# Kernel tuning notes

Hardware: AMD Instinct MI355X
Metric: run time of the kernel (lower is better)

The kernel has to match this reference:

```python
import jax, jax.numpy as jnp
import numpy as np
import math

H_IMG, W_IMG = 800, 1216
STRIDES = [4, 8, 16, 32, 64]
SIZES = [32, 64, 128, 256, 512]
RATIOS = [0.5, 1.0, 2.0]
NUM_PER_LEVEL = [(-(-H_IMG // s)) * (-(-W_IMG // s)) * len(RATIOS) for s in STRIDES]
A_TOTAL = sum(NUM_PER_LEVEL)  # 728973
B = 4
PRE_NMS = 1000   # pre_nms_top_n['testing']
POST_NMS = 1000  # post_nms_top_n['testing']
NMS_TH = 0.7
MIN_SIZE = 1e-3
BBOX_XFORM_CLIP = math.log(1000.0 / 16)
NEG = -1e10
LEVELS_NP = np.repeat(np.arange(len(NUM_PER_LEVEL)), NUM_PER_LEVEL).astype(np.int32)


def _make_anchors():
    out = []
    for stride, size in zip(STRIDES, SIZES):
        fh, fw = -(-H_IMG // stride), -(-W_IMG // stride)
        r = np.sqrt(np.asarray(RATIOS, dtype=np.float64))
        ws, hs = size / r, size * r
        base = np.stack([-ws / 2, -hs / 2, ws / 2, hs / 2], axis=1)  # [3,4]
        sx = np.arange(fw, dtype=np.float64) * stride
        sy = np.arange(fh, dtype=np.float64) * stride
        gy, gx = np.meshgrid(sy, sx, indexing='ij')
        shifts = np.stack([gx.ravel(), gy.ravel(), gx.ravel(), gy.ravel()], axis=1)
        out.append((shifts[:, None, :] + base[None]).reshape(-1, 4))
    return np.concatenate(out, 0).astype(np.float32)


def setup_inputs() -> dict:
    key = jax.random.key(0)
    k1, k2 = jax.random.split(key)
    objectness = jax.random.normal(k1, (B, A_TOTAL), dtype=jnp.float32)
    deltas = jax.random.normal(k2, (B, A_TOTAL, 4), dtype=jnp.float32) * 0.2
    anchors = jnp.asarray(_make_anchors())
    return {'objectness': objectness, 'deltas': deltas, 'anchors': anchors}


def _decode(deltas, anchors):
    # BoxCoder.decode with weights (1,1,1,1)
    wa = anchors[:, 2] - anchors[:, 0]
    ha = anchors[:, 3] - anchors[:, 1]
    cxa = anchors[:, 0] + 0.5 * wa
    cya = anchors[:, 1] + 0.5 * ha
    dx, dy = deltas[..., 0], deltas[..., 1]
    dw = jnp.minimum(deltas[..., 2], BBOX_XFORM_CLIP)
    dh = jnp.minimum(deltas[..., 3], BBOX_XFORM_CLIP)
    cx = dx * wa + cxa
    cy = dy * ha + cya
    w = jnp.exp(dw) * wa
    h = jnp.exp(dh) * ha
    return jnp.stack([cx - 0.5 * w, cy - 0.5 * h, cx + 0.5 * w, cy + 0.5 * h], axis=-1)


def _topk_per_level(obj):
    # _get_top_n_idx: independent top-k within each anchor level, indices offset
    idxs, off = [], 0
    for n in NUM_PER_LEVEL:
        k = min(PRE_NMS, n)
        _, ti = jax.lax.top_k(obj[:, off:off + n], k)
        idxs.append(ti + off)
        off += n
    return jnp.concatenate(idxs, axis=1)


def _pairwise_iou(b):
    area = (b[:, 2] - b[:, 0]) * (b[:, 3] - b[:, 1])
    lt = jnp.maximum(b[:, None, :2], b[None, :, :2])
    rb = jnp.minimum(b[:, None, 2:], b[None, :, 2:])
    wh = jnp.clip(rb - lt, 0.0)
    inter = wh[..., 0] * wh[..., 1]
    return inter / (area[:, None] + area[None, :] - inter)


def _filter_image(boxes, scores, lvl):
    # clip_boxes_to_image
    x1 = jnp.clip(boxes[:, 0], 0.0, W_IMG)
    y1 = jnp.clip(boxes[:, 1], 0.0, H_IMG)
    x2 = jnp.clip(boxes[:, 2], 0.0, W_IMG)
    y2 = jnp.clip(boxes[:, 3], 0.0, H_IMG)
    boxes = jnp.stack([x1, y1, x2, y2], axis=1)
    # remove_small_boxes (as a validity mask; fixed shapes under jit)
    valid = ((x2 - x1) >= MIN_SIZE) & ((y2 - y1) >= MIN_SIZE)
    scores = jnp.where(valid, scores, NEG)
    N = boxes.shape[0]
    # batched_nms: offset boxes per level so levels never overlap
    sg_boxes = jax.lax.stop_gradient(boxes)
    offset = lvl.astype(boxes.dtype) * (sg_boxes.max() + 1.0)
    order = jnp.argsort(-jax.lax.stop_gradient(scores))
    iou = _pairwise_iou(sg_boxes[order] + offset[order][:, None])  # [N,N]
    idx = jnp.arange(N)
    def body(i, keep):
        sup = (iou[i] > NMS_TH) & keep[i] & (idx > i)
        return keep & ~sup
    keep = jax.lax.fori_loop(0, N, body, valid[order])
    # kept entries in score order, then truncate to POST_NMS (fixed shape)
    prio = jnp.where(keep, idx, N)
    sel = jnp.argsort(prio)[:POST_NMS]
    kept = keep[sel]
    src = order[sel]
    out_b = jnp.where(kept[:, None], boxes[src], 0.0)
    out_s = jnp.where(kept, scores[src], NEG)
    return out_b, out_s


def reference(objectness, deltas, anchors):
    proposals = _decode(deltas, anchors)                      # [B,A,4]
    top_idx = _topk_per_level(objectness)                     # [B,5000]
    obj_sel = jnp.take_along_axis(objectness, top_idx, axis=1)
    prop_sel = jnp.take_along_axis(proposals, top_idx[..., None], axis=1)
    lvl_sel = jnp.asarray(LEVELS_NP)[top_idx]
    boxes, scores = jax.vmap(_filter_image)(prop_sel, obj_sel, lvl_sel)
    return boxes, scores  # [B,POST_NMS,4], [B,POST_NMS]
```

## Files before the change

### kernel.cpp

```cpp
#include <hip/hip_runtime.h>
#include <stdint.h>

#pragma clang fp contract(off)

#define B_IMGS   4
#define NLVL     5
#define A_TOTAL  242991
#define NSEL     4741
#define NBUCK    8192
#define BSHIFT   19
#define CAND_CAP 2048
#define POST_NMS 1000
#define NBL      (B_IMGS * NLVL)
#define NMS_TH   0.7f
#define NEGV     (-1e10f)
#define W_IMGF   1216.0f
#define H_IMGF   800.0f
#define MIN_SZ   1e-3f
#define BBOX_CLIP 4.135166556742356f

#define NSLICE_PER_IMG 34

__device__ __forceinline__ int lvl_k(int l) { return (l == 4) ? 741 : 1000; }

__device__ __forceinline__ unsigned flipf(float f) {
    unsigned u = __float_as_uint(f);
    return u ^ (unsigned)(((int)u >> 31) | 0x80000000);
}
__device__ __forceinline__ float unflipf(unsigned os) {
    unsigned u = (os & 0x80000000u) ? (os ^ 0x80000000u) : ~os;
    return __uint_as_float(u);
}

__device__ __forceinline__ void async_cp16(const void* g, void* l) {
    __builtin_amdgcn_global_load_lds(
        (const __attribute__((address_space(1))) unsigned*)g,
        (__attribute__((address_space(3))) unsigned*)l,
        16, 0, 0);
}

static constexpr size_t OFF_BM    = 0;
static constexpr size_t OFF_CNT   = 128;
static constexpr size_t OFF_DI    = 208;
static constexpr size_t OFF_D2    = 224;
static constexpr size_t OFF_HSL   = 256;
static constexpr size_t OFF_PSL   = OFF_HSL  + (size_t)B_IMGS * NSLICE_PER_IMG * NBUCK * 4;
static constexpr size_t OFF_CAND  = OFF_PSL  + (size_t)B_IMGS * NSLICE_PER_IMG * 256 * 4;
static constexpr size_t OFF_SEL   = OFF_CAND + (size_t)NBL * CAND_CAP * 8;
static constexpr size_t OFF_BOXR  = OFF_SEL  + (size_t)B_IMGS * NSEL * 8;
static constexpr size_t OFF_SCR   = OFF_BOXR + (size_t)B_IMGS * NSEL * 16;
static constexpr size_t OFF_BOXL  = OFF_SCR  + (size_t)B_IMGS * NSEL * 4;
static constexpr size_t OFF_VAL   = OFF_BOXL + (size_t)B_IMGS * NSEL * 16;
static constexpr size_t OFF_RMAP  = OFF_VAL  + (size_t)B_IMGS * NSEL * 4;
static constexpr size_t OFF_KEEP  = OFF_RMAP + (size_t)B_IMGS * NSEL * 4;
static constexpr size_t OFF_MASK  = (OFF_KEEP + (size_t)B_IMGS * NSEL * 4 + 15) & ~(size_t)15;
static constexpr size_t WS_NEED   = OFF_MASK + (size_t)NBL * 1024 * 16 * 8;

#define HBLK_PER_IMG 34
__global__ __launch_bounds__(512) void k_hist(const float* __restrict__ obj,
                                              unsigned* __restrict__ hist_sl,
                                              unsigned* __restrict__ part_sl,
                                              unsigned* __restrict__ cntz) {
    __shared__ __align__(16) unsigned lh[NBUCK];
    const int tid = threadIdx.x;
    const int b = blockIdx.x / HBLK_PER_IMG;
    const int r = blockIdx.x - b * HBLK_PER_IMG;
    if (r == 33) {
        if (b == 0 && tid < 28) cntz[tid] = 0;
        return;
    }
    int sofs, sub, chunk, lstart, n;
    if (r < 24)      { sofs = 0;  sub = r;      chunk = 7600; lstart = 0;      n = 182400; }
    else if (r < 30) { sofs = 24; sub = r - 24; chunk = 7600; lstart = 182400; n = 45600; }
    else if (r < 32) { sofs = 30; sub = r - 30; chunk = 5700; lstart = 228000; n = 11400; }
    else             { sofs = 32; sub = 0;      chunk = 2850; lstart = 239400; n = 2850; }
    #pragma unroll
    for (int i = tid; i < NBUCK; i += 512) lh[i] = 0;
    __syncthreads();
    const int s0 = sub * chunk;
    const int m = min(chunk, n - s0);
    const float* src = obj + (size_t)b * A_TOTAL + lstart + s0;
    const int peel0 = (int)(((16u - ((unsigned)(uintptr_t)src & 15u)) & 15u) >> 2);
    const int peel  = (peel0 < m) ? peel0 : m;
    const int nv    = (m - peel) >> 2;
    const float4* s4 = (const float4*)(src + peel);
    const int tail0 = peel + (nv << 2);
#define H1(f) atomicAdd(&lh[flipf(f) >> BSHIFT], 1u)
#define H4(v) do { H1((v).x); H1((v).y); H1((v).z); H1((v).w); } while (0)
    if (tid < peel) H1(src[tid]);
    for (int i = tid; i < nv; i += 2048) {
        if (i + 1536 < nv) {
            float4 a0 = s4[i], a1 = s4[i + 512], a2 = s4[i + 1024], a3 = s4[i + 1536];
            H4(a0); H4(a1); H4(a2); H4(a3);
        } else {
            float4 a0 = s4[i]; H4(a0);
            if (i + 512  < nv) { float4 a = s4[i + 512];  H4(a); }
            if (i + 1024 < nv) { float4 a = s4[i + 1024]; H4(a); }
        }
    }
    for (int i = tail0 + tid; i < m; i += 512) H1(src[i]);
#undef H4
#undef H1
    __syncthreads();
    const int slice = b * NSLICE_PER_IMG + sofs + sub;
    unsigned* gh = hist_sl + (size_t)slice * NBUCK;
    #pragma unroll
    for (int i = tid; i < NBUCK / 4; i += 512)
        ((uint4*)gh)[i] = ((const uint4*)lh)[i];
    if (tid < 256) {
        unsigned s = 0;
        #pragma unroll
        for (int i = 0; i < 32; ++i) s += lh[tid * 32 + ((i + tid) & 31)];
        part_sl[(size_t)slice * 256 + tid] = s;
    }
}

#define CBLK_PER_IMG 65
__global__ __launch_bounds__(256) void k_compact(const float* __restrict__ obj,
                                                 const unsigned* __restrict__ hist_sl,
                                                 const unsigned* __restrict__ part_sl,
                                                 unsigned* __restrict__ cnt,
                                                 unsigned long long* __restrict__ cand) {
    __shared__ unsigned long long sbuf[CAND_CAP];
    __shared__ unsigned wsum[4];
    __shared__ unsigned fcnt[4];
    __shared__ unsigned s_cum, s_thr, lcnt, gbase;
    const int tid = threadIdx.x;
    const int b = blockIdx.x / CBLK_PER_IMG;
    const int r = blockIdx.x - b * CBLK_PER_IMG;
    int l, sofs, nsub, sub, chunk, lstart, n;
    if (r < 48)      { l = 0; sofs = 0;  nsub = 24; sub = r;      chunk = 3800; lstart = 0;      n = 182400; }
    else if (r < 60) { l = 1; sofs = 24; nsub = 6;  sub = r - 48; chunk = 3800; lstart = 182400; n = 45600; }
    else if (r < 63) { l = 2; sofs = 30; nsub = 2;  sub = r - 60; chunk = 3800; lstart = 228000; n = 11400; }
    else if (r == 63){ l = 3; sofs = 32; nsub = 1;  sub = 0;      chunk = 2850; lstart = 239400; n = 2850; }
    else             { l = 4; sofs = 33; nsub = 0;  sub = 0;      chunk = 741;  lstart = 242250; n = 741; }
    const int bl = b * NLVL + l;
    const int kl = lvl_k(l);
    if (tid == 0) { lcnt = 0; s_cum = 0; }
    __syncthreads();
    unsigned T = 0;
    if (l < 4) {
        const int lane = tid & 63, wv = tid >> 6;
        const unsigned* pb = part_sl + (size_t)(b * NSLICE_PER_IMG + sofs) * 256 + (255 - tid);
        unsigned x = 0;
        #pragma unroll 6
        for (int s = 0; s < nsub; ++s) x += pb[(size_t)s * 256];
        #pragma unroll
        for (int d = 1; d < 64; d <<= 1) {
            unsigned up = __shfl_up(x, d);
            if (lane >= d) x += up;
        }
        if (lane == 63) wsum[wv] = x;
        __syncthreads();
        unsigned add = 0;
        #pragma unroll
        for (int u = 0; u < 3; ++u) if (u < wv) add += wsum[u];
        const unsigned suffix = x + add;
        unsigned long long bm = __ballot(suffix >= (unsigned)kl);
        if (lane == 0) fcnt[wv] = (unsigned)__popcll(bm);
        __syncthreads();
        const int chnk = (int)(fcnt[0] + fcnt[1] + fcnt[2] + fcnt[3]) - 1;
        if ((255 - tid) == chnk + 1) s_cum = suffix;
        __syncthreads();
        if (tid < 64) {
            unsigned y = 0;
            if (tid < 32) {
                const unsigned* hb = hist_sl + (size_t)(b * NSLICE_PER_IMG + sofs) * NBUCK
                                   + chnk * 32 + (31 - tid);
                #pragma unroll 6
                for (int s = 0; s < nsub; ++s) y += hb[(size_t)s * NBUCK];
            }
            #pragma unroll
            for (int d = 1; d < 32; d <<= 1) {
                unsigned up = __shfl_up(y, d);
                if (tid >= d) y += up;
            }
            unsigned suf2 = s_cum + y;
            unsigned long long bm2 = __ballot((tid < 32) && (suf2 >= (unsigned)kl));
            if (tid == 0) {
                int istar = (int)__popcll(bm2) - 1;
                s_thr = (unsigned)(chnk * 32 + istar);
            }
        }
        __syncthreads();
        T = s_thr;
    }
    const int s0 = sub * chunk;
    const int m = min(chunk, n - s0);
    const int abase = lstart + s0;
    const float* src = obj + (size_t)b * A_TOTAL + abase;
    const int peel0 = (int)(((16u - ((unsigned)(uintptr_t)src & 15u)) & 15u) >> 2);
    const int peel  = (peel0 < m) ? peel0 : m;
    const int nv    = (m - peel) >> 2;
    const float4* s4 = (const float4*)(src + peel);
    const int tail0 = peel + (nv << 2);
#define E1(f, idx) do { unsigned os_ = flipf(f); \
    if ((os_ >> BSHIFT) >= T) { \
        unsigned slot = atomicAdd(&lcnt, 1u); \
        if (slot < CAND_CAP) \
            sbuf[slot] = (((unsigned long long)(~os_)) << 32) | (unsigned)(idx); \
    } } while (0)
#define E4(v, gb) do { E1((v).x, (gb)); E1((v).y, (gb) + 1); \
                       E1((v).z, (gb) + 2); E1((v).w, (gb) + 3); } while (0)
    if (tid < peel) E1(src[tid], abase + tid);
    for (int i = tid; i < nv; i += 512) {
        const int gb0 = abase + peel + (i << 2);
        if (i + 256 < nv) {
            float4 a0 = s4[i], a1 = s4[i + 256];
            E4(a0, gb0);
            E4(a1, gb0 + 1024);
        } else {
            float4 a0 = s4[i];
            E4(a0, gb0);
        }
    }
    for (int i = tail0 + tid; i < m; i += 256) E1(src[i], abase + i);
#undef E4
#undef E1
    __syncthreads();
    unsigned total = lcnt; if (total > CAND_CAP) total = CAND_CAP;
    if (tid == 0) gbase = atomicAdd(&cnt[bl], total);
    __syncthreads();
    const unsigned gb = gbase;
    for (unsigned i = tid; i < total; i += 256) {
        unsigned g = gb + i;
        if (g < CAND_CAP)
            cand[(size_t)bl * CAND_CAP + g] = sbuf[i];
    }
}

__device__ __forceinline__ int lbound_lds(const unsigned long long* s, int len,
                                          unsigned long long key) {
    int lo = 0, hi = len;
    while (lo < hi) {
        int mid = (lo + hi) >> 1;
        if (s[mid] < key) lo = mid + 1; else hi = mid;
    }
    return lo;
}

__global__ __launch_bounds__(1024) void k_sortdec(
        const unsigned long long* __restrict__ cand, const unsigned* __restrict__ cnt,
        unsigned long long* __restrict__ sel,
        const float* __restrict__ deltas, const float* __restrict__ anchors,
        float* __restrict__ boxes_r, float* __restrict__ score_r,
        float* __restrict__ boxes_l, int* __restrict__ valid_l,
        int* __restrict__ rankmap, float* __restrict__ boxmax,
        unsigned* __restrict__ done_i) {
    __shared__ __align__(16) char smem[38016];
    __shared__ float wmax[16];
    __shared__ int s_last;
    const int bl = blockIdx.x;
    const int b = bl / NLVL, l = bl - (bl / NLVL) * NLVL;
    const int tid = threadIdx.x;

    {
        unsigned long long* keys = (unsigned long long*)smem;
        int m = (int)cnt[bl];
        if (m > CAND_CAP) m = CAND_CAP;
        for (int i = tid; i < CAND_CAP; i += 1024)
            keys[i] = (i < m) ? cand[(size_t)bl * CAND_CAP + i] : ~0ULL;
        __syncthreads();
        for (int k = 2; k <= CAND_CAP; k <<= 1) {
            for (int j = k >> 1; j > 0; j >>= 1) {
                int i = ((tid / j) * (j << 1)) + (tid % j);
                int p = i + j;
                bool up = ((i & k) == 0);
                unsigned long long a = keys[i], c = keys[p];
                if ((a > c) == up) { keys[i] = c; keys[p] = a; }
                __syncthreads();
            }
        }
        int kl = lvl_k(l);
        for (int q = tid; q < kl; q += 1024)
            sel[(size_t)b * NSEL + l * 1000 + q] = keys[q];
    }
    __syncthreads();
    if (tid == 0) {
        __threadfence();
        unsigned old = __hip_atomic_fetch_add(done_i + b, 1u,
                                              __ATOMIC_ACQ_REL, __HIP_MEMORY_SCOPE_AGENT);
        s_last = (old == NLVL - 1);
        if (old == NLVL - 1) __threadfence();
    }
    __syncthreads();
    if (!s_last) return;

    unsigned long long* skey = (unsigned long long*)smem;
    for (int i = tid; i < NSEL; i += 1024)
        skey[i] = sel[(size_t)b * NSEL + i];
    __syncthreads();
    float mxall = 0.0f;
    for (int sub = 0; sub < 5; ++sub) {
        int p = sub * 1024 + tid;
        bool on = p < NSEL;
        float mx = 0.0f;
        if (on) {
            int l2i = p / 1000;
            int q = p - l2i * 1000;
            unsigned long long key = skey[p];
            unsigned a = (unsigned)(key & 0xFFFFFFFFu);
            unsigned os = ~((unsigned)(key >> 32));
            if (a >= A_TOTAL) a = 0;
            float score = unflipf(os);
            int r = q;
            for (int l2 = 0; l2 < NLVL; ++l2) {
                if (l2 == l2i) continue;
                r += lbound_lds(skey + l2 * 1000, lvl_k(l2), key);
            }
            const float* dv = deltas + ((size_t)b * A_TOTAL + a) * 4;
            const float* av = anchors + (size_t)a * 4;
            float ax1 = av[0], ay1 = av[1], ax2 = av[2], ay2 = av[3];
            float wa = ax2 - ax1, ha = ay2 - ay1;
            float cxa = ax1 + 0.5f * wa, cya = ay1 + 0.5f * ha;
            float dx = dv[0], dy = dv[1];
            float dw = fminf(dv[2], BBOX_CLIP), dh = fminf(dv[3], BBOX_CLIP);
            float cx = dx * wa + cxa, cy = dy * ha + cya;
            float w = expf(dw) * wa, h = expf(dh) * ha;
            float x1 = cx - 0.5f * w, y1 = cy - 0.5f * h;
            float x2 = cx + 0.5f * w, y2 = cy + 0.5f * h;
            float x1c = fminf(fmaxf(x1, 0.0f), W_IMGF);
            float y1c = fminf(fmaxf(y1, 0.0f), H_IMGF);
            float x2c = fminf(fmaxf(x2, 0.0f), W_IMGF);
            float y2c = fminf(fmaxf(y2, 0.0f), H_IMGF);
            int valid = ((x2c - x1c) >= MIN_SZ) && ((y2c - y1c) >= MIN_SZ);
            mx = fmaxf(fmaxf(x1c, y1c), fmaxf(x2c, y2c));
            size_t rp = (size_t)b * NSEL + r;
            boxes_r[rp * 4 + 0] = x1c; boxes_r[rp * 4 + 1] = y1c;
            boxes_r[rp * 4 + 2] = x2c; boxes_r[rp * 4 + 3] = y2c;
            score_r[rp] = score;
            size_t pp = (size_t)b * NSEL + p;
            boxes_l[pp * 4 + 0] = x1c; boxes_l[pp * 4 + 1] = y1c;
            boxes_l[pp * 4 + 2] = x2c; boxes_l[pp * 4 + 3] = y2c;
            valid_l[pp] = valid;
            rankmap[pp] = r;
        }
        mxall = fmaxf(mxall, mx);
    }
    #pragma unroll
    for (int o = 32; o > 0; o >>= 1)
        mxall = fmaxf(mxall, __shfl_xor(mxall, o));
    if ((tid & 63) == 0) wmax[tid >> 6] = mxall;
    __syncthreads();
    if (tid == 0) {
        float m2 = wmax[0];
        #pragma unroll
        for (int i = 1; i < 16; ++i) m2 = fmaxf(m2, wmax[i]);
        boxmax[b] = m2;
    }
}

__global__ void k_mask(const float* __restrict__ boxes_l, const float* __restrict__ boxmax,
                       unsigned long long* __restrict__ mask) {
    int bl = blockIdx.z;
    int b = bl / NLVL, l = bl - b * NLVL;
    int kl = lvl_k(l);
    int w = blockIdx.x, rg = blockIdx.y, tid = threadIdx.x;
    if (rg * 256 >= kl) return;
    float M = boxmax[b] + 1.0f;
    float off = (float)l * M;
    __shared__ float cb[64][5];
    int j0 = w * 64;
    if (tid < 64) {
        int j = j0 + tid;
        if (j < kl) {
            const float* bp = boxes_l + ((size_t)b * NSEL + l * 1000 + j) * 4;
            float x1 = bp[0] + off, y1 = bp[1] + off, x2 = bp[2] + off, y2 = bp[3] + off;
            cb[tid][0] = x1; cb[tid][1] = y1; cb[tid][2] = x2; cb[tid][3] = y2;
            cb[tid][4] = (x2 - x1) * (y2 - y1);
        }
    }
    __syncthreads();
    int i = rg * 256 + tid;
    if (i >= kl) return;
    unsigned long long word = 0;
    if (j0 + 63 > i) {
        const float* bp = boxes_l + ((size_t)b * NSEL + l * 1000 + i) * 4;
        float ix1 = bp[0] + off, iy1 = bp[1] + off, ix2 = bp[2] + off, iy2 = bp[3] + off;
        float ai = (ix2 - ix1) * (iy2 - iy1);
        int jmax = min(64, kl - j0);
        for (int bb = 0; bb < jmax; ++bb) {
            int jj = j0 + bb;
            if (jj <= i) continue;
            float ltx = fmaxf(ix1, cb[bb][0]), lty = fmaxf(iy1, cb[bb][1]);
            float rbx = fminf(ix2, cb[bb][2]), rby = fminf(iy2, cb[bb][3]);
            float ww = fmaxf(rbx - ltx, 0.0f), hh = fmaxf(rby - lty, 0.0f);
            float inter = ww * hh;
            float iou = inter / ((ai + cb[bb][4]) - inter);
            if (iou > NMS_TH) word |= (1ULL << bb);
        }
    }
    mask[((size_t)bl * 1024 + i) * 16 + w] = word;
}

__global__ __launch_bounds__(256) void k_resout(const int* __restrict__ valid_l,
                                                const int* __restrict__ rankmap,
                                                const unsigned long long* __restrict__ mask,
                                                int* __restrict__ keep_r,
                                                unsigned* __restrict__ done2,
                                                const float* __restrict__ boxes_r,
                                                const float* __restrict__ score_r,
                                                float* __restrict__ out) {
    __shared__ __align__(16) unsigned long long sbufA[64 * 16];
    __shared__ __align__(16) unsigned long long sbufB[64 * 16];
    __shared__ int ps[256];
    __shared__ int s_flag;
    const int bl = blockIdx.x;
    const int b = bl / NLVL, l = bl - b * NLVL;
    const int kl = lvl_k(l);
    const int tid = threadIdx.x;
    const int lane = tid & 63;
    const int base = b * NSEL + l * 1000;
    const int nch = (kl + 63) >> 6;
    const char* mbyte = (const char*)(mask + (size_t)bl * 1024 * 16);

    unsigned long long keep_w = 0;
    if (tid < 64) {
        for (int c = 0; c < 16; ++c) {
            int q = c * 64 + lane;
            int vv = (q < kl) ? valid_l[base + q] : 0;
            unsigned long long bm = __ballot(vv);
            if (lane == c) keep_w = bm;
        }
        const char* g0 = mbyte + (size_t)lane * 16;
        #pragma unroll
        for (int j = 0; j < 8; ++j)
            async_cp16(g0 + j * 1024, (char*)sbufA + j * 1024);
    }
    for (int c = 0; c < nch; ++c) {
        __syncthreads();
        if (tid < 64) {
            unsigned long long* cur = (c & 1) ? sbufB : sbufA;
            unsigned long long* nxt = (c & 1) ? sbufA : sbufB;
            if (c + 1 < nch) {
                const char* g1 = mbyte + (size_t)(c + 1) * 8192 + (size_t)lane * 16;
                #pragma unroll
                for (int j = 0; j < 8; ++j)
                    async_cp16(g1 + j * 1024, (char*)nxt + j * 1024);
            }
            unsigned long long kw = __shfl(keep_w, c);
            if (kw) {
                unsigned long long diag = cur[lane * 16 + c];
                unsigned dlo = (unsigned)diag, dhi = (unsigned)(diag >> 32);
                unsigned long long nz = __ballot(diag != 0ULL);
                unsigned long long rem = kw & nz;
                while (rem) {
                    int rr = __ffsll((long long)rem) - 1;
                    unsigned lo = __builtin_amdgcn_readlane(dlo, rr);
                    unsigned hi = __builtin_amdgcn_readlane(dhi, rr);
                    unsigned long long d = ((unsigned long long)hi << 32) | lo;
                    kw &= ~d;
                    rem &= ~(d | (1ULL << rr));
                }
                unsigned long long supp = 0;
                if (lane < 16) {
                    #pragma unroll
                    for (int rr = 0; rr < 64; ++rr) {
                        unsigned long long mm = cur[rr * 16 + lane];
                        supp |= (((kw >> rr) & 1ULL) ? mm : 0ULL);
                    }
                }
                if (lane == c) keep_w = kw;
                else if (lane < 16 && lane > c) keep_w &= ~supp;
            }
        }
    }
    __syncthreads();
    if (tid < 64) {
        for (int c = 0; c < 16; ++c) {
            unsigned long long kwc = __shfl(keep_w, c);
            int q = c * 64 + lane;
            if (q < kl)
                keep_r[b * NSEL + rankmap[base + q]] = (int)((kwc >> lane) & 1ULL);
        }
    }
    __syncthreads();

    if (tid == 0) {
        __threadfence();
        unsigned old = __hip_atomic_fetch_add(done2 + b, 1u,
                                              __ATOMIC_ACQ_REL, __HIP_MEMORY_SCOPE_AGENT);
        s_flag = (old == NLVL - 1);
        if (old == NLVL - 1) __threadfence();
    }
    __syncthreads();
    if (!s_flag) return;

    float* ob = out + (size_t)b * POST_NMS * 4;
    float* osc = out + (size_t)B_IMGS * POST_NMS * 4 + (size_t)b * POST_NMS;
    for (int p = tid; p < POST_NMS; p += 256) {
        ob[p * 4 + 0] = 0.0f; ob[p * 4 + 1] = 0.0f;
        ob[p * 4 + 2] = 0.0f; ob[p * 4 + 3] = 0.0f;
        osc[p] = NEGV;
    }
    __syncthreads();
    const int CH = 19;
    int basei = tid * CH;
    int c0 = 0;
    #pragma unroll
    for (int k = 0; k < CH; ++k) {
        int rr = basei + k;
        if (rr < NSEL) c0 += keep_r[b * NSEL + rr];
    }
    ps[tid] = c0;
    __syncthreads();
    for (int ofs = 1; ofs < 256; ofs <<= 1) {
        int v = (tid >= ofs) ? ps[tid - ofs] : 0;
        __syncthreads();
        ps[tid] += v;
        __syncthreads();
    }
    int p = ps[tid] - c0;
    #pragma unroll
    for (int k = 0; k < CH; ++k) {
        int rr = basei + k;
        if (rr < NSEL && keep_r[b * NSEL + rr]) {
            if (p < POST_NMS) {
                const float* bp = boxes_r + ((size_t)b * NSEL + rr) * 4;
                ob[p * 4 + 0] = bp[0]; ob[p * 4 + 1] = bp[1];
                ob[p * 4 + 2] = bp[2]; ob[p * 4 + 3] = bp[3];
                osc[p] = score_r[(size_t)b * NSEL + rr];
            }
            ++p;
        }
    }
}

extern "C" void kernel_launch(void* const* d_in, const int* in_sizes, int n_in,
                              void* d_out, int out_size, void* d_ws, size_t ws_size,
                              hipStream_t stream) {
    const float* obj     = (const float*)d_in[0];
    const float* deltas  = (const float*)d_in[1];
    const float* anchors = (const float*)d_in[2];
    float* out = (float*)d_out;

    char* ws = (char*)d_ws;
    float*               boxmax  = (float*)(ws + OFF_BM);
    unsigned*            cnt     = (unsigned*)(ws + OFF_CNT);
    unsigned*            done_i  = (unsigned*)(ws + OFF_DI);
    unsigned*            done2   = (unsigned*)(ws + OFF_D2);
    unsigned*            hist_sl = (unsigned*)(ws + OFF_HSL);
    unsigned*            part_sl = (unsigned*)(ws + OFF_PSL);
    unsigned long long*  cand    = (unsigned long long*)(ws + OFF_CAND);
    unsigned long long*  sel     = (unsigned long long*)(ws + OFF_SEL);
    float*               boxes_r = (float*)(ws + OFF_BOXR);
    float*               score_r = (float*)(ws + OFF_SCR);
    float*               boxes_l = (float*)(ws + OFF_BOXL);
    int*                 valid_l = (int*)(ws + OFF_VAL);
    int*                 rankmap = (int*)(ws + OFF_RMAP);
    int*                 keep_r  = (int*)(ws + OFF_KEEP);
    unsigned long long*  maskp   = (unsigned long long*)(ws + OFF_MASK);

    (void)in_sizes; (void)n_in; (void)out_size; (void)ws_size; (void)WS_NEED;

    k_hist<<<B_IMGS * HBLK_PER_IMG, 512, 0, stream>>>(obj, hist_sl, part_sl, cnt);
    k_compact<<<B_IMGS * CBLK_PER_IMG, 256, 0, stream>>>(obj, hist_sl, part_sl, cnt, cand);
    k_sortdec<<<NBL, 1024, 0, stream>>>(cand, cnt, sel, deltas, anchors,
                                        boxes_r, score_r, boxes_l, valid_l,
                                        rankmap, boxmax, done_i);
    k_mask<<<dim3(16, 4, NBL), 256, 0, stream>>>(boxes_l, boxmax, maskp);
    k_resout<<<NBL, 256, 0, stream>>>(valid_l, rankmap, maskp, keep_r, done2,
                                      boxes_r, score_r, out);
}
```

Before: 193.0 us.

## Replace last-block decode with per-image spin barrier splitting decode across five blocks

Before, only the last of the five level blocks per image did the ranking and decode of all ~4741 selected candidates, with five passes per thread. Now all five blocks wait on a per-image spin barrier and each decodes one 1024-wide slice. The per-image box max is written as five partials that k_mask reduces. This relies on all 20 blocks being co-resident for the spin barrier, and on the barrier counter being reset between calls, which is not visible here.

```diff
diff --git a/kernel.cpp b/kernel.cpp
--- a/kernel.cpp
+++ b/kernel.cpp
@@ -39,7 +39,7 @@
         16, 0, 0);
 }
 
-static constexpr size_t OFF_BM    = 0;
+static constexpr size_t OFF_BM5   = 0;
 static constexpr size_t OFF_CNT   = 128;
 static constexpr size_t OFF_DI    = 208;
 static constexpr size_t OFF_D2    = 224;
@@ -245,11 +245,10 @@
         const float* __restrict__ deltas, const float* __restrict__ anchors,
         float* __restrict__ boxes_r, float* __restrict__ score_r,
         float* __restrict__ boxes_l, int* __restrict__ valid_l,
-        int* __restrict__ rankmap, float* __restrict__ boxmax,
-        unsigned* __restrict__ done_i) {
+        int* __restrict__ rankmap, unsigned* __restrict__ boxmax5,
+        unsigned* __restrict__ bar_i) {
     __shared__ __align__(16) char smem[38016];
     __shared__ float wmax[16];
-    __shared__ int s_last;
     const int bl = blockIdx.x;
     const int b = bl / NLVL, l = bl - (bl / NLVL) * NLVL;
     const int tid = threadIdx.x;
@@ -276,88 +275,89 @@
             sel[(size_t)b * NSEL + l * 1000 + q] = keys[q];
     }
     __syncthreads();
+
     if (tid == 0) {
         __threadfence();
-        unsigned old = __hip_atomic_fetch_add(done_i + b, 1u,
-                                              __ATOMIC_ACQ_REL, __HIP_MEMORY_SCOPE_AGENT);
-        s_last = (old == NLVL - 1);
-        if (old == NLVL - 1) __threadfence();
-    }
-    __syncthreads();
-    if (!s_last) return;
+        __hip_atomic_fetch_add(bar_i + b, 1u, __ATOMIC_RELAXED, __HIP_MEMORY_SCOPE_AGENT);
+        while (__hip_atomic_load(bar_i + b, __ATOMIC_RELAXED, __HIP_MEMORY_SCOPE_AGENT)
+               < (unsigned)NLVL)
+            __builtin_amdgcn_s_sleep(2);
+        __threadfence();
+    }
+    __syncthreads();
 
     unsigned long long* skey = (unsigned long long*)smem;
     for (int i = tid; i < NSEL; i += 1024)
         skey[i] = sel[(size_t)b * NSEL + i];
     __syncthreads();
-    float mxall = 0.0f;
-    for (int sub = 0; sub < 5; ++sub) {
-        int p = sub * 1024 + tid;
-        bool on = p < NSEL;
-        float mx = 0.0f;
-        if (on) {
-            int l2i = p / 1000;
-            int q = p - l2i * 1000;
-            unsigned long long key = skey[p];
-            unsigned a = (unsigned)(key & 0xFFFFFFFFu);
-            unsigned os = ~((unsigned)(key >> 32));
-            if (a >= A_TOTAL) a = 0;
-            float score = unflipf(os);
-            int r = q;
-            for (int l2 = 0; l2 < NLVL; ++l2) {
-                if (l2 == l2i) continue;
-                r += lbound_lds(skey + l2 * 1000, lvl_k(l2), key);
-            }
-            const float* dv = deltas + ((size_t)b * A_TOTAL + a) * 4;
-            const float* av = anchors + (size_t)a * 4;
-            float ax1 = av[0], ay1 = av[1], ax2 = av[2], ay2 = av[3];
-            float wa = ax2 - ax1, ha = ay2 - ay1;
-            float cxa = ax1 + 0.5f * wa, cya = ay1 + 0.5f * ha;
-            float dx = dv[0], dy = dv[1];
-            float dw = fminf(dv[2], BBOX_CLIP), dh = fminf(dv[3], BBOX_CLIP);
-            float cx = dx * wa + cxa, cy = dy * ha + cya;
-            float w = expf(dw) * wa, h = expf(dh) * ha;
-            float x1 = cx - 0.5f * w, y1 = cy - 0.5f * h;
-            float x2 = cx + 0.5f * w, y2 = cy + 0.5f * h;
-            float x1c = fminf(fmaxf(x1, 0.0f), W_IMGF);
-            float y1c = fminf(fmaxf(y1, 0.0f), H_IMGF);
-            float x2c = fminf(fmaxf(x2, 0.0f), W_IMGF);
-            float y2c = fminf(fmaxf(y2, 0.0f), H_IMGF);
-            int valid = ((x2c - x1c) >= MIN_SZ) && ((y2c - y1c) >= MIN_SZ);
-            mx = fmaxf(fmaxf(x1c, y1c), fmaxf(x2c, y2c));
-            size_t rp = (size_t)b * NSEL + r;
-            boxes_r[rp * 4 + 0] = x1c; boxes_r[rp * 4 + 1] = y1c;
-            boxes_r[rp * 4 + 2] = x2c; boxes_r[rp * 4 + 3] = y2c;
-            score_r[rp] = score;
-            size_t pp = (size_t)b * NSEL + p;
-            boxes_l[pp * 4 + 0] = x1c; boxes_l[pp * 4 + 1] = y1c;
-            boxes_l[pp * 4 + 2] = x2c; boxes_l[pp * 4 + 3] = y2c;
-            valid_l[pp] = valid;
-            rankmap[pp] = r;
-        }
-        mxall = fmaxf(mxall, mx);
+    const int sub = l;
+    int p = sub * 1024 + tid;
+    bool on = p < NSEL;
+    float mx = 0.0f;
+    if (on) {
+        int l2i = p / 1000;
+        int q = p - l2i * 1000;
+        unsigned long long key = skey[p];
+        unsigned a = (unsigned)(key & 0xFFFFFFFFu);
+        unsigned os = ~((unsigned)(key >> 32));
+        if (a >= A_TOTAL) a = 0;
+        float score = unflipf(os);
+        int r = q;
+        for (int l2 = 0; l2 < NLVL; ++l2) {
+            if (l2 == l2i) continue;
+            r += lbound_lds(skey + l2 * 1000, lvl_k(l2), key);
+        }
+        const float* dv = deltas + ((size_t)b * A_TOTAL + a) * 4;
+        const float* av = anchors + (size_t)a * 4;
+        float ax1 = av[0], ay1 = av[1], ax2 = av[2], ay2 = av[3];
+        float wa = ax2 - ax1, ha = ay2 - ay1;
+        float cxa = ax1 + 0.5f * wa, cya = ay1 + 0.5f * ha;
+        float dx = dv[0], dy = dv[1];
+        float dw = fminf(dv[2], BBOX_CLIP), dh = fminf(dv[3], BBOX_CLIP);
+        float cx = dx * wa + cxa, cy = dy * ha + cya;
+        float w = expf(dw) * wa, h = expf(dh) * ha;
+        float x1 = cx - 0.5f * w, y1 = cy - 0.5f * h;
+        float x2 = cx + 0.5f * w, y2 = cy + 0.5f * h;
+        float x1c = fminf(fmaxf(x1, 0.0f), W_IMGF);
+        float y1c = fminf(fmaxf(y1, 0.0f), H_IMGF);
+        float x2c = fminf(fmaxf(x2, 0.0f), W_IMGF);
+        float y2c = fminf(fmaxf(y2, 0.0f), H_IMGF);
+        int valid = ((x2c - x1c) >= MIN_SZ) && ((y2c - y1c) >= MIN_SZ);
+        mx = fmaxf(fmaxf(x1c, y1c), fmaxf(x2c, y2c));
+        size_t rp = (size_t)b * NSEL + r;
+        boxes_r[rp * 4 + 0] = x1c; boxes_r[rp * 4 + 1] = y1c;
+        boxes_r[rp * 4 + 2] = x2c; boxes_r[rp * 4 + 3] = y2c;
+        score_r[rp] = score;
+        size_t pp = (size_t)b * NSEL + p;
+        boxes_l[pp * 4 + 0] = x1c; boxes_l[pp * 4 + 1] = y1c;
+        boxes_l[pp * 4 + 2] = x2c; boxes_l[pp * 4 + 3] = y2c;
+        valid_l[pp] = valid;
+        rankmap[pp] = r;
     }
     #pragma unroll
     for (int o = 32; o > 0; o >>= 1)
-        mxall = fmaxf(mxall, __shfl_xor(mxall, o));
-    if ((tid & 63) == 0) wmax[tid >> 6] = mxall;
+        mx = fmaxf(mx, __shfl_xor(mx, o));
+    if ((tid & 63) == 0) wmax[tid >> 6] = mx;
     __syncthreads();
     if (tid == 0) {
         float m2 = wmax[0];
         #pragma unroll
         for (int i = 1; i < 16; ++i) m2 = fmaxf(m2, wmax[i]);
-        boxmax[b] = m2;
-    }
-}
-
-__global__ void k_mask(const float* __restrict__ boxes_l, const float* __restrict__ boxmax,
+        boxmax5[b * 5 + sub] = __float_as_uint(m2);
+    }
+}
+
+__global__ void k_mask(const float* __restrict__ boxes_l, const unsigned* __restrict__ boxmax5,
                        unsigned long long* __restrict__ mask) {
     int bl = blockIdx.z;
     int b = bl / NLVL, l = bl - b * NLVL;
     int kl = lvl_k(l);
     int w = blockIdx.x, rg = blockIdx.y, tid = threadIdx.x;
     if (rg * 256 >= kl) return;
-    float M = boxmax[b] + 1.0f;
+    float M = __uint_as_float(boxmax5[b * 5 + 0]);
+    #pragma unroll
+    for (int j = 1; j < 5; ++j) M = fmaxf(M, __uint_as_float(boxmax5[b * 5 + j]));
+    M += 1.0f;
     float off = (float)l * M;
     __shared__ float cb[64][5];
     int j0 = w * 64;
@@ -535,9 +535,9 @@
     float* out = (float*)d_out;
 
     char* ws = (char*)d_ws;
-    float*               boxmax  = (float*)(ws + OFF_BM);
+    unsigned*            boxmax5 = (unsigned*)(ws + OFF_BM5);
     unsigned*            cnt     = (unsigned*)(ws + OFF_CNT);
-    unsigned*            done_i  = (unsigned*)(ws + OFF_DI);
+    unsigned*            bar_i   = (unsigned*)(ws + OFF_DI);
     unsigned*            done2   = (unsigned*)(ws + OFF_D2);
     unsigned*            hist_sl = (unsigned*)(ws + OFF_HSL);
     unsigned*            part_sl = (unsigned*)(ws + OFF_PSL);
@@ -557,8 +557,8 @@
     k_compact<<<B_IMGS * CBLK_PER_IMG, 256, 0, stream>>>(obj, hist_sl, part_sl, cnt, cand);
     k_sortdec<<<NBL, 1024, 0, stream>>>(cand, cnt, sel, deltas, anchors,
                                         boxes_r, score_r, boxes_l, valid_l,
-                                        rankmap, boxmax, done_i);
-    k_mask<<<dim3(16, 4, NBL), 256, 0, stream>>>(boxes_l, boxmax, maskp);
+                                        rankmap, boxmax5, bar_i);
+    k_mask<<<dim3(16, 4, NBL), 256, 0, stream>>>(boxes_l, boxmax5, maskp);
     k_resout<<<NBL, 256, 0, stream>>>(valid_l, rankmap, maskp, keep_r, done2,
                                       boxes_r, score_r, out);
 }
```

Result: faster. 180.1 us (-6.7%).
